# Kernel tuning notes

Hardware: AMD Instinct MI355X
Metric: run time of the kernel (lower is better)

Reference implementation:

```python
import jax, jax.numpy as jnp
import numpy as np

N = 100000   # nodes
E = 1600000  # edges
NF = 8       # node features
H = 128      # hid_channel


def _gcn(x, ei, W, b):
    """PyG GCNConv: add self-loops, sym-normalize, x@W then scatter-add, +bias."""
    n = x.shape[0]
    loop = jnp.arange(n)
    s = jnp.concatenate([ei[0], loop])
    d = jnp.concatenate([ei[1], loop])
    deg = jax.ops.segment_sum(jnp.ones_like(s, jnp.float32), d, num_segments=n)
    dinv = jnp.where(deg > 0, jax.lax.rsqrt(deg), 0.0)
    norm = dinv[s] * dinv[d]                       # [E+n]
    xw = x @ W                                     # [n, out]
    out = jax.ops.segment_sum(xw[s] * norm[:, None], d, num_segments=n)
    return out + b


def _dag_pool(x, ei, k):
    """DAGPool(k): contiguous-k mean clustering; unpool restores saved (x, ei)."""
    n = x.shape[0]
    nc = -(-n // k)
    cid = jnp.arange(n) // k
    cnt = jax.ops.segment_sum(jnp.ones((n,), jnp.float32), cid, num_segments=nc)
    xp = jax.ops.segment_sum(x, cid, num_segments=nc) / cnt[:, None]
    return xp, ei // k, (x, ei)


def setup_inputs() -> dict:
    key = jax.random.key(0)
    ks = jax.random.split(key, 24)

    def w(k, i, o):
        return jax.random.normal(k, (i, o), jnp.float32) / np.sqrt(i).astype(np.float32)

    d = {
        "x": jax.random.normal(ks[0], (N, NF), jnp.float32),
        "edge_index": jax.random.randint(ks[1], (E, 2), 0, N, dtype=jnp.int64),
        "c1W": w(ks[2], NF, H),          "c1b": jnp.zeros((H,), jnp.float32),
        "c2W": w(ks[3], H + NF, H),      "c2b": jnp.zeros((H,), jnp.float32),
        "c3W": w(ks[4], H + NF, H),      "c3b": jnp.zeros((H,), jnp.float32),
        "c4W": w(ks[5], H, H),           "c4b": jnp.zeros((H,), jnp.float32),
        "c5W": w(ks[6], H, H),           "c5b": jnp.zeros((H,), jnp.float32),
        "f1W": w(ks[7], 2 * H + NF, H),  "f1b": jnp.zeros((H,), jnp.float32),
        "f2W": w(ks[8], 2 * H, H),       "f2b": jnp.zeros((H,), jnp.float32),
        "f3W": w(ks[9], 2 * H, H),       "f3b": jnp.zeros((H,), jnp.float32),
        "f4W": w(ks[10], H + NF, H),     "f4b": jnp.zeros((H,), jnp.float32),
        "f5W": w(ks[11], H + NF, 1),     "f5b": jnp.zeros((1,), jnp.float32),
    }
    return d


def reference(x, edge_index, c1W, c1b, c2W, c2b, c3W, c3b, c4W, c4b, c5W, c5b,
              f1W, f1b, f2W, f2b, f3W, f3b, f4W, f4b, f5W, f5b):
    ei = edge_index.T  # [2, E]
    x_in = x
    h = jax.nn.relu(_gcn(x, ei, c1W, c1b))
    h = jnp.concatenate([h, x_in], axis=-1)
    h = jax.nn.relu(_gcn(h, ei, c2W, c2b))
    h = jnp.concatenate([x_in, h], axis=-1)            # [N, NF+H]

    xp1, ei1, un1 = _dag_pool(h, ei, 5)
    t = jax.nn.relu(_gcn(xp1, ei1, c3W, c3b))
    t = jax.nn.relu(jnp.concatenate([xp1, t], -1) @ f1W + f1b)
    xp2, ei2, un2 = _dag_pool(t, ei1, 3)
    t = jax.nn.relu(_gcn(xp2, ei2, c4W, c4b))
    t = jax.nn.relu(jnp.concatenate([xp2, t], -1) @ f2W + f2b)
    xp3, ei3, un3 = _dag_pool(t, ei2, 3)
    t = jax.nn.relu(_gcn(xp3, ei3, c5W, c5b))
    t = jax.nn.relu(jnp.concatenate([xp3, t], -1) @ f3W + f3b)
    # unpool chain discards pooled features and restores pre-pool1 state
    xr, _ = un1

    h = jax.nn.relu(xr @ f4W + f4b)
    out = jax.nn.sigmoid(jnp.concatenate([x_in, h], -1) @ f5W + f5b)
    return out.ravel()  # [N], binary (num_classes==2 -> 1 logit)
```

## Files before the change

### kernel.cpp

```cpp
#include <hip/hip_runtime.h>
#include <hip/hip_bf16.h>
#include <math.h>


#define NBUK 256

typedef __attribute__((ext_vector_type(8))) short short8;
typedef __attribute__((ext_vector_type(4))) float f32x4;

__device__ __forceinline__ unsigned short f32_to_bf16_rne(float f) {
    unsigned u = __float_as_uint(f);
    return (unsigned short)((u + 0x7fffu + ((u >> 16) & 1u)) >> 16);
}

__global__ __launch_bounds__(512) void bucket_kernel(
    const int* __restrict__ ei, int* __restrict__ bcnt_pad,
    unsigned* __restrict__ bucket, int E, int N, int cap) {
    constexpr int EPB = 4096;
    __shared__ int lcnt[NBUK];
    __shared__ int lcur[NBUK];
    int e0 = blockIdx.x * EPB;
    int e1 = min(e0 + EPB, E);
    if (threadIdx.x < NBUK) lcnt[threadIdx.x] = 0;
    __syncthreads();
    for (int e = e0 + threadIdx.x; e < e1; e += 512) {
        int2 v = ((const int2*)ei)[e];
        if ((unsigned)v.y < (unsigned)N) {
            int b = (int)(((unsigned long long)(unsigned)v.y * NBUK) / (unsigned)N);
            atomicAdd(&lcnt[b], 1);
        }
    }
    __syncthreads();
    if (threadIdx.x < NBUK)
        lcur[threadIdx.x] = atomicAdd(&bcnt_pad[threadIdx.x * 16], lcnt[threadIdx.x]);
    __syncthreads();
    for (int e = e0 + threadIdx.x; e < e1; e += 512) {
        int2 v = ((const int2*)ei)[e];
        if ((unsigned)v.y < (unsigned)N) {
            int b = (int)(((unsigned long long)(unsigned)v.y * NBUK) / (unsigned)N);
            int pos = atomicAdd(&lcur[b], 1);
            if (pos < cap) {
                unsigned s = ((unsigned)v.x < (unsigned)N) ? (unsigned)v.x : 0u;
                int lo = (b * N + NBUK - 1) >> 8;
                bucket[(size_t)b * cap + pos] = ((unsigned)(v.y - lo) << 17) | s;
            }
        }
    }
}

__global__ __launch_bounds__(1024) void csr_kernel(
    const unsigned* __restrict__ bucket, const int* __restrict__ bcnt_pad,
    const float* __restrict__ x,
    int* __restrict__ cnt, int* __restrict__ rowstart, int* __restrict__ col,
    float* __restrict__ dinv, float* __restrict__ xs,
    unsigned short* __restrict__ Abf2, int N, int cap) {
    __shared__ int lcnt[1024];
    __shared__ int lscan[1024];
    int b = blockIdx.x;
    int lo = (int)(((long long)b * N + NBUK - 1) / NBUK);
    int hi = (int)(((long long)(b + 1) * N + NBUK - 1) / NBUK);
    int range = hi - lo;
    lcnt[threadIdx.x] = 0;
    __syncthreads();
    int n = min(bcnt_pad[b * 16], cap);
    const unsigned* bk = bucket + (size_t)b * cap;
    for (int i = threadIdx.x; i < n; i += 1024)
        atomicAdd(&lcnt[bk[i] >> 17], 1);
    __syncthreads();
    int myc = lcnt[threadIdx.x];
    if ((int)threadIdx.x < range) cnt[lo + threadIdx.x] = myc;
    lscan[threadIdx.x] = myc;
    __syncthreads();
    for (int off = 1; off < 1024; off <<= 1) {
        int y = (threadIdx.x >= off) ? lscan[threadIdx.x - off] : 0;
        __syncthreads();
        lscan[threadIdx.x] += y;
        __syncthreads();
    }
    int colbase = b * cap;
    int excl = lscan[threadIdx.x] - myc;
    if ((int)threadIdx.x < range) rowstart[lo + threadIdx.x] = colbase + excl;
    lcnt[threadIdx.x] = excl;
    __syncthreads();
    for (int i = threadIdx.x; i < n; i += 1024) {
        unsigned u = bk[i];
        int pos = atomicAdd(&lcnt[u >> 17], 1);
        col[(size_t)colbase + pos] = (int)(u & 0x1FFFFu);
    }
    if ((int)threadIdx.x < range) {
        int v = lo + threadIdx.x;
        float dv = rsqrtf((float)(myc + 1));
        dinv[v] = dv;
        const float4* x4 = (const float4*)x;
        float4 a = x4[v * 2], c = x4[v * 2 + 1];
        float4* o = (float4*)xs;
        o[v * 2]     = make_float4(a.x * dv, a.y * dv, a.z * dv, a.w * dv);
        o[v * 2 + 1] = make_float4(c.x * dv, c.y * dv, c.z * dv, c.w * dv);
        unsigned short u[8] = {f32_to_bf16_rne(a.x), f32_to_bf16_rne(a.y),
                               f32_to_bf16_rne(a.z), f32_to_bf16_rne(a.w),
                               f32_to_bf16_rne(c.x), f32_to_bf16_rne(c.y),
                               f32_to_bf16_rne(c.z), f32_to_bf16_rne(c.w)};
        ulonglong2 pk;
        pk.x = (unsigned long long)u[0] | ((unsigned long long)u[1] << 16)
             | ((unsigned long long)u[2] << 32) | ((unsigned long long)u[3] << 48);
        pk.y = (unsigned long long)u[4] | ((unsigned long long)u[5] << 16)
             | ((unsigned long long)u[6] << 32) | ((unsigned long long)u[7] << 48);
        *(ulonglong2*)&Abf2[(size_t)v * 160] = pk;
        ulonglong2 z; z.x = 0ull; z.y = 0ull;
        *(ulonglong2*)&Abf2[(size_t)v * 160 + 136] = z;
        *(ulonglong2*)&Abf2[(size_t)v * 160 + 144] = z;
        *(ulonglong2*)&Abf2[(size_t)v * 160 + 152] = z;
    }
}

__global__ __launch_bounds__(256) void agg8_kernel(const float* __restrict__ xs,
                                                   const int* __restrict__ rowstart,
                                                   const int* __restrict__ cnt,
                                                   const int* __restrict__ col,
                                                   const float* __restrict__ dinv,
                                                   float* __restrict__ aggx,
                                                   unsigned short* __restrict__ Abf,
                                                   int n) {
    int g = threadIdx.x >> 3;
    int l = threadIdx.x & 7;
    int v = blockIdx.x * 32 + g;
    if (v >= n) return;
    int start = rowstart[v];
    int m = cnt[v];
    float ax = 0.f;
    for (int base = 0; base < m; base += 8) {
        int mm = min(m - base, 8);
        int si = (l < mm) ? col[start + base + l] : 0;
#pragma unroll 8
        for (int t = 0; t < 8; t++) {
            if (t < mm) {
                int s = __shfl(si, t, 8);
                ax += xs[(size_t)s * 8 + l];
            }
        }
    }
    ax += xs[(size_t)v * 8 + l];
    float dv = dinv[v];
    ax *= dv;
    aggx[(size_t)v * 8 + l] = ax;
    Abf[(size_t)v * 160 + 128 + l] = f32_to_bf16_rne(ax);
#pragma unroll 3
    for (int t = l; t < 24; t += 8) Abf[(size_t)v * 160 + 136 + t] = 0;
}

__global__ __launch_bounds__(256) void agg128_kernel(const unsigned* __restrict__ rows,
                                                     const int* __restrict__ rowstart,
                                                     const int* __restrict__ cnt,
                                                     const int* __restrict__ col,
                                                     const float* __restrict__ dinv,
                                                     unsigned short* __restrict__ Abf,
                                                     int n) {
    int v = blockIdx.x * 4 + (threadIdx.x >> 6);
    int lane = threadIdx.x & 63;
    if (v >= n) return;
    float ax = 0.f, ay = 0.f;
    int start = rowstart[v];
    int end = start + cnt[v];
    for (int base = start; base < end; base += 64) {
        int m = end - base; if (m > 64) m = 64;
        int si = (lane < m) ? col[base + lane] : 0;
        int t = 0;
        for (; t + 8 <= m; t += 8) {
            int s0 = __shfl(si, t),     s1 = __shfl(si, t + 1);
            int s2 = __shfl(si, t + 2), s3 = __shfl(si, t + 3);
            int s4 = __shfl(si, t + 4), s5 = __shfl(si, t + 5);
            int s6 = __shfl(si, t + 6), s7 = __shfl(si, t + 7);
            unsigned u0 = rows[(size_t)s0 * 64 + lane];
            unsigned u1 = rows[(size_t)s1 * 64 + lane];
            unsigned u2 = rows[(size_t)s2 * 64 + lane];
            unsigned u3 = rows[(size_t)s3 * 64 + lane];
            unsigned u4 = rows[(size_t)s4 * 64 + lane];
            unsigned u5 = rows[(size_t)s5 * 64 + lane];
            unsigned u6 = rows[(size_t)s6 * 64 + lane];
            unsigned u7 = rows[(size_t)s7 * 64 + lane];
            ax += (__uint_as_float(u0 << 16) + __uint_as_float(u1 << 16))
                + (__uint_as_float(u2 << 16) + __uint_as_float(u3 << 16))
                + (__uint_as_float(u4 << 16) + __uint_as_float(u5 << 16))
                + (__uint_as_float(u6 << 16) + __uint_as_float(u7 << 16));
            ay += (__uint_as_float(u0 & 0xffff0000u) + __uint_as_float(u1 & 0xffff0000u))
                + (__uint_as_float(u2 & 0xffff0000u) + __uint_as_float(u3 & 0xffff0000u))
                + (__uint_as_float(u4 & 0xffff0000u) + __uint_as_float(u5 & 0xffff0000u))
                + (__uint_as_float(u6 & 0xffff0000u) + __uint_as_float(u7 & 0xffff0000u));
        }
        for (; t + 4 <= m; t += 4) {
            int s0 = __shfl(si, t),     s1 = __shfl(si, t + 1);
            int s2 = __shfl(si, t + 2), s3 = __shfl(si, t + 3);
            unsigned u0 = rows[(size_t)s0 * 64 + lane];
            unsigned u1 = rows[(size_t)s1 * 64 + lane];
            unsigned u2 = rows[(size_t)s2 * 64 + lane];
            unsigned u3 = rows[(size_t)s3 * 64 + lane];
            ax += (__uint_as_float(u0 << 16) + __uint_as_float(u1 << 16))
                + (__uint_as_float(u2 << 16) + __uint_as_float(u3 << 16));
            ay += (__uint_as_float(u0 & 0xffff0000u) + __uint_as_float(u1 & 0xffff0000u))
                + (__uint_as_float(u2 & 0xffff0000u) + __uint_as_float(u3 & 0xffff0000u));
        }
        for (; t < m; t++) {
            int s = __shfl(si, t);
            unsigned u = rows[(size_t)s * 64 + lane];
            ax += __uint_as_float(u << 16);
            ay += __uint_as_float(u & 0xffff0000u);
        }
    }
    unsigned us = rows[(size_t)v * 64 + lane];
    ax += __uint_as_float(us << 16);
    ay += __uint_as_float(us & 0xffff0000u);
    float dv = dinv[v];
    unsigned pk = (unsigned)f32_to_bf16_rne(ax * dv)
                | ((unsigned)f32_to_bf16_rne(ay * dv) << 16);
    ((unsigned*)Abf)[(size_t)v * 80 + lane] = pk;
}

__global__ __launch_bounds__(256) void gemm8_kernel(
    const float* __restrict__ A1, const float* __restrict__ W,
    const float* __restrict__ bias, const float* __restrict__ dinv,
    unsigned short* __restrict__ out, int n) {
    constexpr int K = 8, KP = 12, NPB = 32;
    __shared__ float lds[NPB * KP];
    int node0 = blockIdx.x * NPB;
    for (int idx = threadIdx.x; idx < NPB * K; idx += 256) {
        int r = idx / K, k = idx - r * K;
        int node = node0 + r;
        lds[r * KP + k] = (node < n) ? A1[(size_t)node * K + k] : 0.f;
    }
    __syncthreads();
    int f8 = threadIdx.x & 15, ng = threadIdx.x >> 4;
    int fbase = f8 * 8;
    float acc[2][8];
#pragma unroll
    for (int r = 0; r < 2; r++)
#pragma unroll
        for (int j = 0; j < 8; j++) acc[r][j] = 0.f;
    for (int k = 0; k < K; k += 4) {
        float4 wlo[4], whi[4];
#pragma unroll
        for (int kk = 0; kk < 4; kk++) {
            wlo[kk] = *(const float4*)&W[(size_t)(k + kk) * 128 + fbase];
            whi[kk] = *(const float4*)&W[(size_t)(k + kk) * 128 + fbase + 4];
        }
#pragma unroll
        for (int r = 0; r < 2; r++) {
            float4 a = *(const float4*)&lds[(2 * ng + r) * KP + k];
            float av[4] = {a.x, a.y, a.z, a.w};
#pragma unroll
            for (int kk = 0; kk < 4; kk++) {
                acc[r][0] += av[kk] * wlo[kk].x; acc[r][1] += av[kk] * wlo[kk].y;
                acc[r][2] += av[kk] * wlo[kk].z; acc[r][3] += av[kk] * wlo[kk].w;
                acc[r][4] += av[kk] * whi[kk].x; acc[r][5] += av[kk] * whi[kk].y;
                acc[r][6] += av[kk] * whi[kk].z; acc[r][7] += av[kk] * whi[kk].w;
            }
        }
    }
    float4 blo = *(const float4*)&bias[fbase];
    float4 bhi = *(const float4*)&bias[fbase + 4];
    float bv[8] = {blo.x, blo.y, blo.z, blo.w, bhi.x, bhi.y, bhi.z, bhi.w};
#pragma unroll
    for (int r = 0; r < 2; r++) {
        int node = node0 + 2 * ng + r;
        if (node < n) {
            float dv = dinv[node];
            unsigned short u[8];
#pragma unroll
            for (int j = 0; j < 8; j++)
                u[j] = f32_to_bf16_rne(fmaxf(acc[r][j] + bv[j], 0.f) * dv);
            ulonglong2 pk;
            pk.x = (unsigned long long)u[0] | ((unsigned long long)u[1] << 16)
                 | ((unsigned long long)u[2] << 32) | ((unsigned long long)u[3] << 48);
            pk.y = (unsigned long long)u[4] | ((unsigned long long)u[5] << 16)
                 | ((unsigned long long)u[6] << 32) | ((unsigned long long)u[7] << 48);
            *(ulonglong2*)&out[(size_t)node * 128 + fbase] = pk;
        }
    }
}

__global__ __launch_bounds__(256) void pack_w_kernel(const float* __restrict__ W1,
                                                     const float* __restrict__ W2,
                                                     unsigned short* __restrict__ wp1,
                                                     unsigned short* __restrict__ wp2) {
    int tt = blockIdx.x * 256 + threadIdx.x;
    const float* W = (tt < 20480) ? W1 : W2;
    unsigned short* wp = (tt < 20480) ? wp1 : wp2;
    int t = (tt < 20480) ? tt : tt - 20480;
    if (t >= 20480) return;
    int i = t & 7, l = (t >> 3) & 63, fc = (t >> 9) & 7, ks = t >> 12;
    int k = ks * 32 + (l >> 4) * 8 + i;
    int c = (l & 15) + 16 * fc;
    float v = (k < 136) ? W[(size_t)k * 128 + c] : 0.f;
    wp[t] = f32_to_bf16_rne(v);
}

template <int MODE>
__global__ __launch_bounds__(256) void mfma_gemm(
    const unsigned short* __restrict__ A, const unsigned short* __restrict__ wp,
    const float* __restrict__ bias, const float* __restrict__ x,
    const float* __restrict__ f5W, const float* __restrict__ f5b,
    void* __restrict__ outv, int n) {
    __shared__ float ldsx[64];
    int node0 = blockIdx.x * 64;
    if constexpr (MODE == 2) {
        if (threadIdx.x < 64) {
            int rc = min(node0 + (int)threadIdx.x, n - 1);
            float s = 0.f;
#pragma unroll
            for (int k = 0; k < 8; k++) s += x[(size_t)rc * 8 + k] * f5W[k];
            ldsx[threadIdx.x] = s;
        }
        __syncthreads();
    }
    int wave = threadIdx.x >> 6, lane = threadIdx.x & 63;
    int g = lane >> 4, r = lane & 15;
    int row0 = node0 + wave * 16;
    int arow = min(row0 + r, n - 1);

    short8 a[5];
#pragma unroll
    for (int ks = 0; ks < 5; ks++)
        a[ks] = *(const short8*)&A[(size_t)arow * 160 + ks * 32 + g * 8];

    f32x4 acc[8] = {};
#pragma unroll
    for (int ks = 0; ks < 5; ks++) {
#pragma unroll
        for (int fc = 0; fc < 8; fc++) {
            short8 w = *(const short8*)&wp[(size_t)((ks * 8 + fc) * 64 + lane) * 8];
            acc[fc] = __builtin_amdgcn_mfma_f32_16x16x32_bf16(a[ks], w, acc[fc], 0, 0, 0);
        }
    }

    if constexpr (MODE == 1) {
        unsigned short* out = (unsigned short*)outv;
#pragma unroll
        for (int fc = 0; fc < 8; fc++) {
            int c = r + 16 * fc;
            float bc = bias[c];
#pragma unroll
            for (int v = 0; v < 4; v++) {
                int row = row0 + 4 * g + v;
                if (row < n)
                    out[(size_t)row * 160 + 8 + c] =
                        f32_to_bf16_rne(fmaxf(acc[fc][v] + bc, 0.f));
            }
        }
    } else {
        float plog[4] = {0.f, 0.f, 0.f, 0.f};
#pragma unroll
        for (int fc = 0; fc < 8; fc++) {
            int c = r + 16 * fc;
            float bc = bias[c];
            float w5 = f5W[8 + c];
#pragma unroll
            for (int v = 0; v < 4; v++)
                plog[v] += fmaxf(acc[fc][v] + bc, 0.f) * w5;
        }
#pragma unroll
        for (int m = 1; m < 16; m <<= 1) {
#pragma unroll
            for (int v = 0; v < 4; v++) plog[v] += __shfl_xor(plog[v], m);
        }
        if (r == 0) {
            float* out = (float*)outv;
            float fb = f5b[0];
#pragma unroll
            for (int v = 0; v < 4; v++) {
                int row = row0 + 4 * g + v;
                if (row < n)
                    out[row] = 1.f / (1.f + expf(-(plog[v] + ldsx[wave * 16 + 4 * g + v] + fb)));
            }
        }
    }
}

extern "C" void kernel_launch(void* const* d_in, const int* in_sizes, int n_in,
                              void* d_out, int out_size, void* d_ws, size_t ws_size,
                              hipStream_t stream) {
    const float* x   = (const float*)d_in[0];
    const int*   ei  = (const int*)d_in[1];
    const float* c1W = (const float*)d_in[2];
    const float* c1b = (const float*)d_in[3];
    const float* c2W = (const float*)d_in[4];
    const float* c2b = (const float*)d_in[5];
    const float* f4W = (const float*)d_in[18];
    const float* f4b = (const float*)d_in[19];
    const float* f5W = (const float*)d_in[20];
    const float* f5b = (const float*)d_in[21];
    float* out = (float*)d_out;

    int N = in_sizes[0] / 8;
    int E = in_sizes[1] / 2;

    char* p = (char*)d_ws;
    auto alloc = [&](size_t bytes) {
        char* q = p;
        p += (bytes + 255) & ~(size_t)255;
        return q;
    };
    const int cap = 8192;
    int*            cnt      = (int*)alloc((size_t)N * 4);
    int*            rowstart = (int*)alloc((size_t)N * 4);
    int*            bcnt_pad = (int*)alloc(NBUK * 16 * 4);
    float*          dinv     = (float*)alloc((size_t)N * 4);
    int*            col      = (int*)alloc((size_t)NBUK * cap * 4);
    float*          xs       = (float*)alloc((size_t)N * 8 * 4);
    float*          aggx     = (float*)alloc((size_t)N * 8 * 4);
    unsigned short* bufH1    = (unsigned short*)alloc((size_t)N * 128 * 2);
    unsigned short* Abf      = (unsigned short*)alloc((size_t)N * 160 * 2);
    unsigned short* Abf2     = (unsigned short*)alloc((size_t)N * 160 * 2);
    unsigned short* wp2      = (unsigned short*)alloc(20480 * 2);
    unsigned short* wp4      = (unsigned short*)alloc(20480 * 2);

    unsigned* bucket = (unsigned*)bufH1;

    (void)hipMemsetAsync(bcnt_pad, 0, NBUK * 16 * 4, stream);

    pack_w_kernel<<<160, 256, 0, stream>>>(c2W, f4W, wp2, wp4);

    int gB = (E + 4095) / 4096;
    bucket_kernel<<<gB, 512, 0, stream>>>(ei, bcnt_pad, bucket, E, N, cap);

    csr_kernel<<<NBUK, 1024, 0, stream>>>(bucket, bcnt_pad, x, cnt, rowstart, col,
                                          dinv, xs, Abf2, N, cap);

    agg8_kernel<<<(N + 31) / 32, 256, 0, stream>>>(xs, rowstart, cnt, col, dinv,
                                                   aggx, Abf, N);

    gemm8_kernel<<<(N + 31) / 32, 256, 0, stream>>>(aggx, c1W, c1b, dinv, bufH1, N);

    agg128_kernel<<<(N + 3) / 4, 256, 0, stream>>>((const unsigned*)bufH1, rowstart,
                                                   cnt, col, dinv, Abf, N);

    int g64 = (N + 63) / 64;
    mfma_gemm<1><<<g64, 256, 0, stream>>>(Abf, wp2, c2b, nullptr, nullptr, nullptr,
                                          Abf2, N);
    mfma_gemm<2><<<g64, 256, 0, stream>>>(Abf2, wp4, f4b, x, f5W, f5b, out, N);
}
```

Baseline: 189.6 us.

## Fuse conv2 GEMM and f4/f5 head GEMM into one kernel via LDS

Merges the two MFMA GEMM kernels into one. The ReLU output of the conv2 GEMM is written as bf16 into an LDS tile together with the bf16 copy of x, then reloaded as the A operand of the f4 GEMM and fed into the f5 sigmoid epilogue. This removes the global Abf2 buffer (about 32MB of writes and reads), one kernel launch, and the csr_kernel stores that filled Abf2. In exchange each block uses about 21KB of LDS and a barrier, and holds more live registers across the two GEMMs.

Result: faster. 169.0 us (-10.9%).

```diff
diff --git a/kernel.cpp b/kernel.cpp
--- a/kernel.cpp
+++ b/kernel.cpp
@@ -52,8 +52,7 @@
     const unsigned* __restrict__ bucket, const int* __restrict__ bcnt_pad,
     const float* __restrict__ x,
     int* __restrict__ cnt, int* __restrict__ rowstart, int* __restrict__ col,
-    float* __restrict__ dinv, float* __restrict__ xs,
-    unsigned short* __restrict__ Abf2, int N, int cap) {
+    float* __restrict__ dinv, float* __restrict__ xs, int N, int cap) {
     __shared__ int lcnt[1024];
     __shared__ int lscan[1024];
     int b = blockIdx.x;
@@ -96,20 +95,6 @@
         float4* o = (float4*)xs;
         o[v * 2]     = make_float4(a.x * dv, a.y * dv, a.z * dv, a.w * dv);
         o[v * 2 + 1] = make_float4(c.x * dv, c.y * dv, c.z * dv, c.w * dv);
-        unsigned short u[8] = {f32_to_bf16_rne(a.x), f32_to_bf16_rne(a.y),
-                               f32_to_bf16_rne(a.z), f32_to_bf16_rne(a.w),
-                               f32_to_bf16_rne(c.x), f32_to_bf16_rne(c.y),
-                               f32_to_bf16_rne(c.z), f32_to_bf16_rne(c.w)};
-        ulonglong2 pk;
-        pk.x = (unsigned long long)u[0] | ((unsigned long long)u[1] << 16)
-             | ((unsigned long long)u[2] << 32) | ((unsigned long long)u[3] << 48);
-        pk.y = (unsigned long long)u[4] | ((unsigned long long)u[5] << 16)
-             | ((unsigned long long)u[6] << 32) | ((unsigned long long)u[7] << 48);
-        *(ulonglong2*)&Abf2[(size_t)v * 160] = pk;
-        ulonglong2 z; z.x = 0ull; z.y = 0ull;
-        *(ulonglong2*)&Abf2[(size_t)v * 160 + 136] = z;
-        *(ulonglong2*)&Abf2[(size_t)v * 160 + 144] = z;
-        *(ulonglong2*)&Abf2[(size_t)v * 160 + 152] = z;
     }
 }
 
@@ -293,24 +278,34 @@
     wp[t] = f32_to_bf16_rne(v);
 }
 
-template <int MODE>
-__global__ __launch_bounds__(256) void mfma_gemm(
-    const unsigned short* __restrict__ A, const unsigned short* __restrict__ wp,
-    const float* __restrict__ bias, const float* __restrict__ x,
+__global__ __launch_bounds__(256) void mfma_fused(
+    const unsigned short* __restrict__ A, const unsigned short* __restrict__ wp2,
+    const float* __restrict__ c2b, const unsigned short* __restrict__ wp4,
+    const float* __restrict__ f4b, const float* __restrict__ x,
     const float* __restrict__ f5W, const float* __restrict__ f5b,
-    void* __restrict__ outv, int n) {
+    float* __restrict__ out, int n) {
+    constexpr int LDH = 168;
+    __shared__ unsigned short lds2[64 * LDH];
     __shared__ float ldsx[64];
     int node0 = blockIdx.x * 64;
-    if constexpr (MODE == 2) {
-        if (threadIdx.x < 64) {
-            int rc = min(node0 + (int)threadIdx.x, n - 1);
-            float s = 0.f;
-#pragma unroll
-            for (int k = 0; k < 8; k++) s += x[(size_t)rc * 8 + k] * f5W[k];
-            ldsx[threadIdx.x] = s;
-        }
-        __syncthreads();
-    }
+
+    if (threadIdx.x < 64) {
+        int row = threadIdx.x;
+        int rc = min(node0 + row, n - 1);
+        const float* xr = &x[(size_t)rc * 8];
+        unsigned short* lr = &lds2[row * LDH];
+        float s = 0.f;
+#pragma unroll
+        for (int k = 0; k < 8; k++) {
+            float xv = xr[k];
+            s += xv * f5W[k];
+            lr[k] = f32_to_bf16_rne(xv);
+        }
+#pragma unroll
+        for (int k = 136; k < 160; k++) lr[k] = 0;
+        ldsx[row] = s;
+    }
+
     int wave = threadIdx.x >> 6, lane = threadIdx.x & 63;
     int g = lane >> 4, r = lane & 15;
     int row0 = node0 + wave * 16;
@@ -326,50 +321,61 @@
     for (int ks = 0; ks < 5; ks++) {
 #pragma unroll
         for (int fc = 0; fc < 8; fc++) {
-            short8 w = *(const short8*)&wp[(size_t)((ks * 8 + fc) * 64 + lane) * 8];
+            short8 w = *(const short8*)&wp2[(size_t)((ks * 8 + fc) * 64 + lane) * 8];
             acc[fc] = __builtin_amdgcn_mfma_f32_16x16x32_bf16(a[ks], w, acc[fc], 0, 0, 0);
         }
     }
 
-    if constexpr (MODE == 1) {
-        unsigned short* out = (unsigned short*)outv;
+#pragma unroll
+    for (int fc = 0; fc < 8; fc++) {
+        int c = r + 16 * fc;
+        float bc = c2b[c];
+#pragma unroll
+        for (int v = 0; v < 4; v++) {
+            int trow = wave * 16 + 4 * g + v;
+            lds2[trow * LDH + 8 + c] = f32_to_bf16_rne(fmaxf(acc[fc][v] + bc, 0.f));
+        }
+    }
+    __syncthreads();
+
+    int trow = wave * 16 + r;
+    short8 a2[5];
+#pragma unroll
+    for (int ks = 0; ks < 5; ks++)
+        a2[ks] = *(const short8*)&lds2[trow * LDH + ks * 32 + g * 8];
+
+    f32x4 acc2[8] = {};
+#pragma unroll
+    for (int ks = 0; ks < 5; ks++) {
 #pragma unroll
         for (int fc = 0; fc < 8; fc++) {
-            int c = r + 16 * fc;
-            float bc = bias[c];
-#pragma unroll
-            for (int v = 0; v < 4; v++) {
-                int row = row0 + 4 * g + v;
-                if (row < n)
-                    out[(size_t)row * 160 + 8 + c] =
-                        f32_to_bf16_rne(fmaxf(acc[fc][v] + bc, 0.f));
-            }
-        }
-    } else {
-        float plog[4] = {0.f, 0.f, 0.f, 0.f};
-#pragma unroll
-        for (int fc = 0; fc < 8; fc++) {
-            int c = r + 16 * fc;
-            float bc = bias[c];
-            float w5 = f5W[8 + c];
-#pragma unroll
-            for (int v = 0; v < 4; v++)
-                plog[v] += fmaxf(acc[fc][v] + bc, 0.f) * w5;
-        }
-#pragma unroll
-        for (int m = 1; m < 16; m <<= 1) {
-#pragma unroll
-            for (int v = 0; v < 4; v++) plog[v] += __shfl_xor(plog[v], m);
-        }
-        if (r == 0) {
-            float* out = (float*)outv;
-            float fb = f5b[0];
-#pragma unroll
-            for (int v = 0; v < 4; v++) {
-                int row = row0 + 4 * g + v;
-                if (row < n)
-                    out[row] = 1.f / (1.f + expf(-(plog[v] + ldsx[wave * 16 + 4 * g + v] + fb)));
-            }
+            short8 w = *(const short8*)&wp4[(size_t)((ks * 8 + fc) * 64 + lane) * 8];
+            acc2[fc] = __builtin_amdgcn_mfma_f32_16x16x32_bf16(a2[ks], w, acc2[fc], 0, 0, 0);
+        }
+    }
+
+    float plog[4] = {0.f, 0.f, 0.f, 0.f};
+#pragma unroll
+    for (int fc = 0; fc < 8; fc++) {
+        int c = r + 16 * fc;
+        float bc = f4b[c];
+        float w5 = f5W[8 + c];
+#pragma unroll
+        for (int v = 0; v < 4; v++)
+            plog[v] += fmaxf(acc2[fc][v] + bc, 0.f) * w5;
+    }
+#pragma unroll
+    for (int m = 1; m < 16; m <<= 1) {
+#pragma unroll
+        for (int v = 0; v < 4; v++) plog[v] += __shfl_xor(plog[v], m);
+    }
+    if (r == 0) {
+        float fb = f5b[0];
+#pragma unroll
+        for (int v = 0; v < 4; v++) {
+            int row = row0 + 4 * g + v;
+            if (row < n)
+                out[row] = 1.f / (1.f + expf(-(plog[v] + ldsx[wave * 16 + 4 * g + v] + fb)));
         }
     }
 }
@@ -408,7 +414,6 @@
     float*          aggx     = (float*)alloc((size_t)N * 8 * 4);
     unsigned short* bufH1    = (unsigned short*)alloc((size_t)N * 128 * 2);
     unsigned short* Abf      = (unsigned short*)alloc((size_t)N * 160 * 2);
-    unsigned short* Abf2     = (unsigned short*)alloc((size_t)N * 160 * 2);
     unsigned short* wp2      = (unsigned short*)alloc(20480 * 2);
     unsigned short* wp4      = (unsigned short*)alloc(20480 * 2);
 
@@ -422,7 +427,7 @@
     bucket_kernel<<<gB, 512, 0, stream>>>(ei, bcnt_pad, bucket, E, N, cap);
 
     csr_kernel<<<NBUK, 1024, 0, stream>>>(bucket, bcnt_pad, x, cnt, rowstart, col,
-                                          dinv, xs, Abf2, N, cap);
+                                          dinv, xs, N, cap);
 
     agg8_kernel<<<(N + 31) / 32, 256, 0, stream>>>(xs, rowstart, cnt, col, dinv,
                                                    aggx, Abf, N);
@@ -432,8 +437,6 @@
     agg128_kernel<<<(N + 3) / 4, 256, 0, stream>>>((const unsigned*)bufH1, rowstart,
                                                    cnt, col, dinv, Abf, N);
 
-    int g64 = (N + 63) / 64;
-    mfma_gemm<1><<<g64, 256, 0, stream>>>(Abf, wp2, c2b, nullptr, nullptr, nullptr,
-                                          Abf2, N);
-    mfma_gemm<2><<<g64, 256, 0, stream>>>(Abf2, wp4, f4b, x, f5W, f5b, out, N);
-}
+    mfma_fused<<<(N + 63) / 64, 256, 0, stream>>>(Abf, wp2, c2b, wp4, f4b, x,
+                                                  f5W, f5b, out, N);
+}
```
